# Kernel optimization log

Hardware: AMD Instinct MI355X
Metric: run time of the kernel (lower is better)

## Reference

```python
import jax, jax.numpy as jnp
import numpy as np

D_MODEL = 1024
N_HEADS = 16
D_HEAD = D_MODEL // N_HEADS
EPS = 1e-5


def setup_inputs() -> dict:
    key = jax.random.key(0)
    ks = jax.random.split(key, 7)
    B, T = 4, 2048
    s = 1.0 / np.sqrt(D_MODEL)
    return {
        "x": jax.random.normal(ks[0], (B, T, D_MODEL), dtype=jnp.float32),
        "ln_g": jnp.ones((D_MODEL,), jnp.float32),
        "ln_b": jnp.zeros((D_MODEL,), jnp.float32),
        "W_qkv": jax.random.normal(ks[1], (D_MODEL, 3 * D_MODEL), jnp.float32) * s,
        "b_qkv": jnp.zeros((3 * D_MODEL,), jnp.float32),
        "W_gate": jax.random.normal(ks[2], (D_MODEL, D_MODEL), jnp.float32) * s,
        "b_gate": jnp.zeros((D_MODEL,), jnp.float32),
        "W_proj": jax.random.normal(ks[3], (D_MODEL, D_MODEL), jnp.float32) * s,
        "b_proj": jnp.zeros((D_MODEL,), jnp.float32),
    }


def _forward(x, ln_g, ln_b, W_qkv, b_qkv, W_gate, b_gate, W_proj, b_proj):
    B, T, D = x.shape
    H, d = N_HEADS, D_HEAD
    # LayerNorm (eps=1e-5, biased variance as in torch)
    mu = jnp.mean(x, axis=-1, keepdims=True)
    var = jnp.mean((x - mu) ** 2, axis=-1, keepdims=True)
    x_norm = (x - mu) * jax.lax.rsqrt(var + EPS) * ln_g + ln_b
    qkv = x_norm @ W_qkv + b_qkv
    q, k, v = jnp.split(qkv, 3, axis=-1)  # each [B,T,D]
    # concept gate uses raw x
    gate = jax.nn.sigmoid(x @ W_gate + b_gate)
    gate = gate / (jnp.mean(gate, axis=-1, keepdims=True) + EPS)
    q = (q * gate).reshape(B, T, H, d)
    k = (k * gate).reshape(B, T, H, d)
    v = v.reshape(B, T, H, d)
    # ReLU^2 feature map in fp32
    q = jax.nn.relu(q.astype(jnp.float32)) ** 2 + EPS
    k = jax.nn.relu(k.astype(jnp.float32)) ** 2 + EPS
    v = v.astype(jnp.float32)
    # causal linear attention via kv recurrence (scan over T, T-major)
    qT = jnp.transpose(q, (1, 0, 2, 3))  # [T,B,H,d]
    kT = jnp.transpose(k, (1, 0, 2, 3))
    vT = jnp.transpose(v, (1, 0, 2, 3))

    def step(carry, inp):
        kv_s, k_s = carry  # [B,H,d,d], [B,H,d]
        q_t, k_t, v_t = inp  # [B,H,d]
        kv_s = kv_s + k_t[..., :, None] * v_t[..., None, :]
        k_s = k_s + k_t
        num = jnp.einsum('bhd,bhdm->bhm', q_t, kv_s)
        den = jnp.einsum('bhd,bhd->bh', q_t, k_s)[..., None] + EPS
        return (kv_s, k_s), num / den

    init = (jnp.zeros((B, H, d, d), jnp.float32), jnp.zeros((B, H, d), jnp.float32))
    _, outT = jax.lax.scan(step, init, (qT, kT, vT))  # [T,B,H,d]
    out = jnp.transpose(outT, (1, 0, 2, 3)).astype(x.dtype).reshape(B, T, D)
    return out @ W_proj + b_proj


def reference(x, ln_g, ln_b, W_qkv, b_qkv, W_gate, b_gate, W_proj, b_proj):
    return _forward(x, ln_g, ln_b, W_qkv, b_qkv, W_gate, b_gate, W_proj, b_proj)
```

## Files before the change

### kernel.cpp

```cpp
#include <hip/hip_runtime.h>
#include <math.h>

#define TOK 8192
#define DM 1024
#define EPSF 1e-5f

typedef __attribute__((ext_vector_type(8))) short short8;
typedef __attribute__((ext_vector_type(4))) float f32x4;

static __device__ __forceinline__ ushort f2bf(float f) {
  unsigned u = __float_as_uint(f);
  unsigned r = (u + 0x7fffu + ((u >> 16) & 1u)) >> 16;
  return (ushort)r;
}
static __device__ __forceinline__ float bf2f(ushort u) {
  return __uint_as_float((unsigned)u << 16);
}

static __device__ __forceinline__ void gload_lds16(const ushort* g, ushort* l) {
  __builtin_amdgcn_global_load_lds((const __attribute__((address_space(1))) void*)g,
                                   (__attribute__((address_space(3))) void*)l, 16, 0, 0);
}

static __device__ __forceinline__ int cswz(int row) {
  return (((row & 7) ^ ((row >> 3) & 7)) << 3);
}

__global__ __launch_bounds__(256) void lncvt_k(const float* __restrict__ x,
                                               const float* __restrict__ g,
                                               const float* __restrict__ b,
                                               ushort* __restrict__ x_b,
                                               ushort* __restrict__ xn_b) {
  __shared__ float red[8];
  int row = blockIdx.x;
  const float4* xr = (const float4*)(x + (size_t)row * DM);
  float4 v = xr[threadIdx.x];
  ushort4 xb4;
  xb4.x = f2bf(v.x); xb4.y = f2bf(v.y); xb4.z = f2bf(v.z); xb4.w = f2bf(v.w);
  ((ushort4*)(x_b + (size_t)row * DM))[threadIdx.x] = xb4;
  float s = v.x + v.y + v.z + v.w;
#pragma unroll
  for (int o = 32; o > 0; o >>= 1) s += __shfl_down(s, o, 64);
  int lane = threadIdx.x & 63, w = threadIdx.x >> 6;
  if (lane == 0) red[w] = s;
  __syncthreads();
  float mu = (red[0] + red[1] + red[2] + red[3]) * (1.0f / DM);
  float dx = v.x - mu, dy = v.y - mu, dz = v.z - mu, dw = v.w - mu;
  float ss = dx * dx + dy * dy + dz * dz + dw * dw;
#pragma unroll
  for (int o = 32; o > 0; o >>= 1) ss += __shfl_down(ss, o, 64);
  if (lane == 0) red[4 + w] = ss;
  __syncthreads();
  float var = (red[4] + red[5] + red[6] + red[7]) * (1.0f / DM);
  float rstd = rsqrtf(var + EPSF);
  float4 gg = ((const float4*)g)[threadIdx.x];
  float4 bb = ((const float4*)b)[threadIdx.x];
  ushort4 o4;
  o4.x = f2bf(dx * rstd * gg.x + bb.x);
  o4.y = f2bf(dy * rstd * gg.y + bb.y);
  o4.z = f2bf(dz * rstd * gg.z + bb.z);
  o4.w = f2bf(dw * rstd * gg.w + bb.w);
  ((ushort4*)(xn_b + (size_t)row * DM))[threadIdx.x] = o4;
}

__global__ __launch_bounds__(256) void tconv_all_k(
    const float* __restrict__ Wg, const float* __restrict__ Wq,
    const float* __restrict__ Wp, ushort* __restrict__ Wtg,
    ushort* __restrict__ Wtq, ushort* __restrict__ Wtp) {
  __shared__ ushort tile[32][33];
  int bid = blockIdx.x;
  const float* W; ushort* Wt; int N; int local;
  if (bid < 1024)      { W = Wg; Wt = Wtg; N = 1024; local = bid; }
  else if (bid < 4096) { W = Wq; Wt = Wtq; N = 3072; local = bid - 1024; }
  else                 { W = Wp; Wt = Wtp; N = 1024; local = bid - 4096; }
  int ntiles = N >> 5;
  int n0 = (local % ntiles) * 32, k0 = (local / ntiles) * 32;
  int tx = threadIdx.x & 31, ty = threadIdx.x >> 5;
#pragma unroll
  for (int i = 0; i < 4; i++) {
    int k = ty + i * 8;
    tile[k][tx] = f2bf(W[(size_t)(k0 + k) * N + n0 + tx]);
  }
  __syncthreads();
#pragma unroll
  for (int i = 0; i < 4; i++) {
    int n = ty + i * 8;
    Wt[(size_t)(n0 + n) * 1024 + k0 + tx] = tile[tx][n];
  }
}

__global__ __launch_bounds__(256) void rowinv_k(const ushort* __restrict__ gate_b,
                                                float* __restrict__ ginv) {
  int row = blockIdx.x * 4 + (threadIdx.x >> 6);
  int l = threadIdx.x & 63;
  const short8* gr = (const short8*)(gate_b + (size_t)row * DM);
  short8 g0 = gr[l * 2], g1 = gr[l * 2 + 1];
  float s = 0.f;
#pragma unroll
  for (int j = 0; j < 8; j++) s += bf2f((ushort)g0[j]) + bf2f((ushort)g1[j]);
#pragma unroll
  for (int o = 1; o < 64; o <<= 1) s += __shfl_xor(s, o, 64);
  if (l == 0) ginv[row] = 1.0f / (s * (1.0f / DM) + EPSF);
}

#define BM 128
#define BN 128
#define BK 64

static __device__ __forceinline__ void stage_tile128(
    const ushort* __restrict__ A, const ushort* __restrict__ Bt,
    int m0, int n0, int k0, int K, ushort* As, ushort* Bs, int w, int lane) {
#pragma unroll
  for (int j = 0; j < 4; j++) {
    int lu = (w * 4 + j) * 64 + lane;
    int r = lu >> 3;
    int kb = (lu & 7) ^ (r & 7);
    gload_lds16(A + (size_t)(m0 + r) * K + k0 + kb * 8, As + (w * 4 + j) * 512);
    gload_lds16(Bt + (size_t)(n0 + r) * K + k0 + kb * 8, Bs + (w * 4 + j) * 512);
  }
}

static __device__ __forceinline__ void compute_tile128(
    const ushort* as, const ushort* bs, int wr, int wc, int lane, f32x4 acc[4][4]) {
#pragma unroll
  for (int ks = 0; ks < 2; ks++) {
    short8 af[4], bfr[4];
    int kq = ks * 4 + (lane >> 4);
#pragma unroll
    for (int f = 0; f < 4; f++) {
      int ra = wr * 64 + f * 16 + (lane & 15);
      af[f] = *(const short8*)&as[(ra * 8 + (kq ^ (ra & 7))) * 8];
      int rb = wc * 64 + f * 16 + (lane & 15);
      bfr[f] = *(const short8*)&bs[(rb * 8 + (kq ^ (rb & 7))) * 8];
    }
#pragma unroll
    for (int i = 0; i < 4; i++)
#pragma unroll
      for (int j2 = 0; j2 < 4; j2++)
        acc[i][j2] = __builtin_amdgcn_mfma_f32_16x16x32_bf16(af[i], bfr[j2], acc[i][j2], 0, 0, 0);
  }
}

#define GEMM_LOOP128(A_, B_, m0_, n0_, K_)                                       \
  f32x4 acc[4][4] = {};                                                          \
  stage_tile128(A_, B_, m0_, n0_, 0, K_, sh, sh + 16384, w, lane);               \
  int nt = (K_) / BK;                                                            \
  for (int t = 0; t < nt; t++) {                                                 \
    __syncthreads();                                                             \
    if (t + 1 < nt)                                                              \
      stage_tile128(A_, B_, m0_, n0_, (t + 1) * BK, K_,                          \
                    sh + ((t + 1) & 1) * 8192, sh + 16384 + ((t + 1) & 1) * 8192,\
                    w, lane);                                                    \
    compute_tile128(sh + (t & 1) * 8192, sh + 16384 + (t & 1) * 8192,            \
                    wr, wc, lane, acc);                                          \
  }                                                                              \
  __syncthreads();

__global__ __launch_bounds__(256) void gemm_bf16_k(
    const ushort* __restrict__ A, const ushort* __restrict__ Bt,
    const float* __restrict__ bias, float* __restrict__ Cf,
    ushort* __restrict__ Cb, int ldc, int K, int mode) {
  __shared__ __align__(16) ushort sh[32768];
  int tid = threadIdx.x, lane = tid & 63, w = tid >> 6;
  int m0 = blockIdx.y * BM, n0 = blockIdx.x * BN;
  int wr = w >> 1, wc = w & 1;
  GEMM_LOOP128(A, Bt, m0, n0, K)
#pragma unroll
  for (int i = 0; i < 4; i++) {
#pragma unroll
    for (int j2 = 0; j2 < 4; j2++) {
      int col = n0 + wc * 64 + j2 * 16 + (lane & 15);
      float bv = bias[col];
#pragma unroll
      for (int r = 0; r < 4; r++) {
        int row = m0 + wr * 64 + i * 16 + (lane >> 4) * 4 + r;
        float v = acc[i][j2][r] + bv;
        if (mode == 2) {
          v = 1.0f / (1.0f + __expf(-v));
          Cb[(size_t)row * ldc + col] = f2bf(v);
        } else {
          Cf[(size_t)row * ldc + col] = v;
        }
      }
    }
  }
}

__global__ __launch_bounds__(256) void gemm_qkv_k(
    const ushort* __restrict__ A, const ushort* __restrict__ Bt,
    const float* __restrict__ bias, const ushort* __restrict__ gate_b,
    const float* __restrict__ ginv,
    ushort* __restrict__ qb, ushort* __restrict__ kb,
    ushort* __restrict__ kt, ushort* __restrict__ vt, int K) {
  __shared__ __align__(16) ushort sh[32768];
  __shared__ float ginvs[128];
  int tid = threadIdx.x, lane = tid & 63, w = tid >> 6;
  int m0 = blockIdx.y * BM, n0 = blockIdx.x * BN;
  int wr = w >> 1, wc = w & 1;
  GEMM_LOOP128(A, Bt, m0, n0, K)
  int region = n0 >> 10;
  int n0b = n0 & 1023;
  int h0 = n0b >> 6;
  if (region < 2) {
    if (tid < 128) ginvs[tid] = ginv[m0 + tid];
#pragma unroll
    for (int it = 0; it < 8; it++) {
      int e = it * 256 + tid;
      int row = e >> 4, ch = e & 15;
      *(short8*)&sh[row * 132 + ch * 8] =
          *(const short8*)&gate_b[(size_t)(m0 + row) * DM + n0b + ch * 8];
    }
    __syncthreads();
#pragma unroll
    for (int i = 0; i < 4; i++) {
#pragma unroll
      for (int j2 = 0; j2 < 4; j2++) {
        int cl = wc * 64 + j2 * 16 + (lane & 15);
        float bv = bias[n0 + cl];
        int rl0 = wr * 64 + i * 16 + (lane >> 4) * 4;
#pragma unroll
        for (int r = 0; r < 4; r++) {
          float gv = bf2f(sh[(rl0 + r) * 132 + cl]) * ginvs[rl0 + r];
          float v = (acc[i][j2][r] + bv) * gv;
          v = fmaxf(v, 0.0f);
          acc[i][j2][r] = v * v + EPSF;
        }
      }
    }
    __syncthreads();
  } else {
#pragma unroll
    for (int i = 0; i < 4; i++)
#pragma unroll
      for (int j2 = 0; j2 < 4; j2++) {
        int cl = wc * 64 + j2 * 16 + (lane & 15);
        float bv = bias[n0 + cl];
#pragma unroll
        for (int r = 0; r < 4; r++) acc[i][j2][r] += bv;
      }
  }
#pragma unroll
  for (int i = 0; i < 4; i++) {
#pragma unroll
    for (int j2 = 0; j2 < 4; j2++) {
      int cl = wc * 64 + j2 * 16 + (lane & 15);
      int rl0 = wr * 64 + i * 16 + (lane >> 4) * 4;
#pragma unroll
      for (int r = 0; r < 4; r++) {
        int row = rl0 + r;
        sh[row * 128 + (cl ^ cswz(row))] = f2bf(acc[i][j2][r]);
      }
    }
  }
  __syncthreads();
  if (region < 2) {
    ushort* dstRM = (region == 0) ? qb : kb;
#pragma unroll
    for (int it = 0; it < 8; it++) {
      int e = it * 256 + tid;
      int row = e >> 4, ch = e & 15;
      short8 val = *(const short8*)&sh[row * 128 + ((ch * 8) ^ cswz(row))];
      int tglob = m0 + row;
      size_t bh2 = (size_t)(tglob >> 11) * 16 + h0 + (ch >> 3);
      *(short8*)&dstRM[(bh2 * 2048 + (tglob & 2047)) * 64 + (ch & 7) * 8] = val;
    }
  }
  if (region >= 1) {
    ushort* dstT = (region == 1) ? kt : vt;
#pragma unroll
    for (int it = 0; it < 8; it++) {
      int e = it * 256 + tid;
      int tch = e & 15, dkrow = e >> 4;
      short8 val;
#pragma unroll
      for (int j = 0; j < 8; j++) {
        int row = tch * 8 + j;
        val[j] = (short)sh[row * 128 + (dkrow ^ cswz(row))];
      }
      int tglob0 = m0 + tch * 8;
      size_t bh2 = (size_t)(tglob0 >> 11) * 16 + h0 + (dkrow >> 6);
      *(short8*)&dstT[(bh2 * 64 + (dkrow & 63)) * 2048 + (tglob0 & 2047)] = val;
    }
  }
}

__global__ __launch_bounds__(256) void chunkpfx_k(const ushort* __restrict__ kt,
                                                  const ushort* __restrict__ vt,
                                                  ushort* __restrict__ KVb,
                                                  float* __restrict__ ksum) {
  int bid = blockIdx.x;
  int bh = (bid & 7) | ((bid >> 5) << 3);
  int dvs = (bid >> 3) & 3;
  int tid = threadIdx.x, l = tid & 63, w = tid >> 6;
  int lg = l >> 4;
  const ushort* vT = vt + ((size_t)bh * 64 + dvs * 16 + (l & 15)) * 2048;
  const ushort* kT = kt + ((size_t)bh * 64 + w * 16 + (l & 15)) * 2048;
  f32x4 run = {0.f, 0.f, 0.f, 0.f};
  float runks = 0.0f;
  short8 a0 = *(const short8*)&vT[lg * 8];
  short8 a1 = *(const short8*)&vT[32 + lg * 8];
  short8 b0 = *(const short8*)&kT[lg * 8];
  short8 b1 = *(const short8*)&kT[32 + lg * 8];
  for (int c = 0; c < 32; c++) {
    ushort* dst = KVb + ((size_t)bh * 32 + c) * 4096 +
                  (size_t)(dvs * 16 + lg * 4) * 64 + w * 16 + (l & 15);
    dst[0] = f2bf(run[0]); dst[64] = f2bf(run[1]);
    dst[128] = f2bf(run[2]); dst[192] = f2bf(run[3]);
    if (dvs == 0) {
      float s = 0.f;
#pragma unroll
      for (int j = 0; j < 8; j++) s += bf2f((ushort)b0[j]) + bf2f((ushort)b1[j]);
      s += __shfl_xor(s, 16, 64);
      s += __shfl_xor(s, 32, 64);
      if (l < 16) ksum[((size_t)bh * 32 + c) * 64 + w * 16 + l] = runks;
      runks += s;
    }
    int cn = (c + 1) & 31;
    short8 na0 = *(const short8*)&vT[cn * 64 + lg * 8];
    short8 na1 = *(const short8*)&vT[cn * 64 + 32 + lg * 8];
    short8 nb0 = *(const short8*)&kT[cn * 64 + lg * 8];
    short8 nb1 = *(const short8*)&kT[cn * 64 + 32 + lg * 8];
    run = __builtin_amdgcn_mfma_f32_16x16x32_bf16(a0, b0, run, 0, 0, 0);
    run = __builtin_amdgcn_mfma_f32_16x16x32_bf16(a1, b1, run, 0, 0, 0);
    a0 = na0; a1 = na1; b0 = nb0; b1 = nb1;
  }
}

__global__ __launch_bounds__(256) void attn_k(
    const ushort* __restrict__ qb, const ushort* __restrict__ kb,
    const ushort* __restrict__ vt, const ushort* __restrict__ KVb,
    const float* __restrict__ ks, ushort* __restrict__ attnout) {
  int c = blockIdx.x, bh = blockIdx.y;
  int b = bh >> 4, h = bh & 15;
  const ushort* qB = qb + ((size_t)bh * 2048 + (size_t)c * 64) * 64;
  const ushort* kB = kb + ((size_t)bh * 2048 + (size_t)c * 64) * 64;
  const ushort* vT = vt + (size_t)bh * 64 * 2048 + (size_t)c * 64;
  const ushort* kvB = KVb + ((size_t)bh * 32 + c) * 4096;
  const float* ksP = ks + ((size_t)bh * 32 + c) * 64;
  __shared__ __align__(16) char SL[64 * 128];
  __shared__ float denp[4][64];
  __shared__ float den2p[4][64];
  __shared__ float invden[64];
  int tid = threadIdx.x, l = tid & 63, w = tid >> 6;
  int lr = l & 15, lg = l >> 4;
  {
    short8 q0 = *(const short8*)&qB[(size_t)l * 64 + w * 16];
    short8 q1 = *(const short8*)&qB[(size_t)l * 64 + w * 16 + 8];
    float d2 = 0.0f;
#pragma unroll
    for (int j = 0; j < 8; j++) {
      d2 += bf2f((ushort)q0[j]) * ksP[w * 16 + j];
      d2 += bf2f((ushort)q1[j]) * ksP[w * 16 + 8 + j];
    }
    den2p[w][l] = d2;
  }
#pragma unroll
  for (int n = 0; n < 4; n++) {
    f32x4 sa = {0.f, 0.f, 0.f, 0.f};
#pragma unroll
    for (int g = 0; g < 2; g++) {
      short8 a = *(const short8*)&kB[(size_t)(w * 16 + lr) * 64 + g * 32 + lg * 8];
      short8 bq = *(const short8*)&qB[(size_t)(n * 16 + lr) * 64 + g * 32 + lg * 8];
      sa = __builtin_amdgcn_mfma_f32_16x16x32_bf16(a, bq, sa, 0, 0, 0);
    }
    int t = n * 16 + lr;
    int s0 = w * 16 + lg * 4;
    float dsum = 0.0f;
    ushort sb[4];
#pragma unroll
    for (int r = 0; r < 4; r++) {
      float v = (s0 + r <= t) ? sa[r] : 0.0f;
      dsum += v;
      sb[r] = f2bf(v);
    }
    dsum += __shfl_xor(dsum, 16, 64);
    dsum += __shfl_xor(dsum, 32, 64);
    if (l < 16) denp[w][n * 16 + l] = dsum;
    int u = (s0 >> 3) ^ (t & 7);
    uint2 p;
    p.x = sb[0] | ((unsigned)sb[1] << 16);
    p.y = sb[2] | ((unsigned)sb[3] << 16);
    *(uint2*)&SL[t * 128 + u * 16 + (s0 & 7) * 2] = p;
  }
  __syncthreads();
  if (tid < 64) {
    float den = denp[0][tid] + denp[1][tid] + denp[2][tid] + denp[3][tid] +
                den2p[0][tid] + den2p[1][tid] + den2p[2][tid] + den2p[3][tid] + EPSF;
    invden[tid] = 1.0f / den;
  }
  __syncthreads();
#pragma unroll
  for (int n = 0; n < 4; n++) {
    f32x4 oa = {0.f, 0.f, 0.f, 0.f};
#pragma unroll
    for (int g = 0; g < 2; g++) {
      short8 a = *(const short8*)&kvB[(size_t)(w * 16 + lr) * 64 + g * 32 + lg * 8];
      short8 bq = *(const short8*)&qB[(size_t)(n * 16 + lr) * 64 + g * 32 + lg * 8];
      oa = __builtin_amdgcn_mfma_f32_16x16x32_bf16(a, bq, oa, 0, 0, 0);
    }
    int t = n * 16 + lr;
#pragma unroll
    for (int g = 0; g < 2; g++) {
      short8 a = *(const short8*)&vT[(size_t)(w * 16 + lr) * 2048 + g * 32 + lg * 8];
      int u = (g * 4 + lg) ^ (t & 7);
      short8 bs = *(const short8*)&SL[t * 128 + u * 16];
      oa = __builtin_amdgcn_mfma_f32_16x16x32_bf16(a, bs, oa, 0, 0, 0);
    }
    float iv = invden[t];
    ushort ob[4];
#pragma unroll
    for (int r = 0; r < 4; r++) ob[r] = f2bf(oa[r] * iv);
    size_t tok = (size_t)b * 2048 + (size_t)c * 64 + t;
    uint2 p;
    p.x = ob[0] | ((unsigned)ob[1] << 16);
    p.y = ob[2] | ((unsigned)ob[3] << 16);
    *(uint2*)&attnout[tok * 1024 + h * 64 + w * 16 + lg * 4] = p;
  }
}

extern "C" void kernel_launch(void* const* d_in, const int* in_sizes, int n_in,
                              void* d_out, int out_size, void* d_ws, size_t ws_size,
                              hipStream_t stream) {
  const float* x      = (const float*)d_in[0];
  const float* ln_g   = (const float*)d_in[1];
  const float* ln_b   = (const float*)d_in[2];
  const float* W_qkv  = (const float*)d_in[3];
  const float* b_qkv  = (const float*)d_in[4];
  const float* W_gate = (const float*)d_in[5];
  const float* b_gate = (const float*)d_in[6];
  const float* W_proj = (const float*)d_in[7];
  const float* b_proj = (const float*)d_in[8];
  float* out = (float*)d_out;

  char* wsb = (char*)d_ws;
  const size_t TD = (size_t)TOK * DM;
  const size_t SLOT = TD * 2;
  ushort* x_b     = (ushort*)(wsb + 0 * SLOT);
  ushort* attnout = (ushort*)(wsb + 0 * SLOT);
  ushort* xn_b    = (ushort*)(wsb + 1 * SLOT);
  ushort* qb      = (ushort*)(wsb + 2 * SLOT);
  ushort* kb      = (ushort*)(wsb + 3 * SLOT);
  ushort* kt      = (ushort*)(wsb + 4 * SLOT);
  ushort* vt      = (ushort*)(wsb + 5 * SLOT);
  ushort* gate_b  = (ushort*)(wsb + 6 * SLOT);
  ushort* Wt_qkv  = (ushort*)(wsb + 8 * SLOT);
  ushort* Wt_gate = (ushort*)(wsb + 8 * SLOT + (size_t)8 * 1024 * 1024);
  ushort* KVb     = (ushort*)(wsb + 8 * SLOT);
  ushort* Wt_proj = (ushort*)(wsb + 9 * SLOT);
  float*  ksum    = (float*)(wsb + 9 * SLOT + (size_t)8 * 1024 * 1024);
  float*  ginv    = (float*)(wsb + 9 * SLOT + (size_t)12 * 1024 * 1024);

  lncvt_k<<<TOK, 256, 0, stream>>>(x, ln_g, ln_b, x_b, xn_b);
  tconv_all_k<<<5120, 256, 0, stream>>>(W_gate, W_qkv, W_proj, Wt_gate, Wt_qkv, Wt_proj);
  gemm_bf16_k<<<dim3(DM / BN, TOK / BM), 256, 0, stream>>>(x_b, Wt_gate, b_gate, nullptr,
                                                           gate_b, DM, DM, 2);
  rowinv_k<<<TOK / 4, 256, 0, stream>>>(gate_b, ginv);
  gemm_qkv_k<<<dim3(3 * DM / BN, TOK / BM), 256, 0, stream>>>(xn_b, Wt_qkv, b_qkv, gate_b,
                                                              ginv, qb, kb, kt, vt, DM);
  chunkpfx_k<<<256, 256, 0, stream>>>(kt, vt, KVb, ksum);
  attn_k<<<dim3(32, 64), 256, 0, stream>>>(qb, kb, vt, KVb, ksum, attnout);
  gemm_bf16_k<<<dim3(DM / BN, TOK / BM), 256, 0, stream>>>(attnout, Wt_proj, b_proj, out,
                                                           nullptr, DM, DM, 0);
}
```

Before: 194.8 us.

## Merge prep kernels and fuse gate row-sum into gate GEMM epilogue

Combines the layernorm/convert kernel and the weight transpose kernel into one launch. It also removes the separate row-inverse kernel: the gate GEMM epilogue now reduces partial row sums of the sigmoid outputs per column block into a small buffer, and the QKV GEMM sums the 8 partials to form the inverse mean. This drops two launches and a re-read of the bf16 gate matrix. In exchange it adds shuffle and LDS reduction work to the gate GEMM epilogue, and the sum is now taken over fp32 sigmoid values rather than bf16-rounded ones.

```diff
diff --git a/kernel.cpp b/kernel.cpp
--- a/kernel.cpp
+++ b/kernel.cpp
@@ -26,81 +26,66 @@
   return (((row & 7) ^ ((row >> 3) & 7)) << 3);
 }
 
-__global__ __launch_bounds__(256) void lncvt_k(const float* __restrict__ x,
-                                               const float* __restrict__ g,
-                                               const float* __restrict__ b,
-                                               ushort* __restrict__ x_b,
-                                               ushort* __restrict__ xn_b) {
-  __shared__ float red[8];
-  int row = blockIdx.x;
-  const float4* xr = (const float4*)(x + (size_t)row * DM);
-  float4 v = xr[threadIdx.x];
-  ushort4 xb4;
-  xb4.x = f2bf(v.x); xb4.y = f2bf(v.y); xb4.z = f2bf(v.z); xb4.w = f2bf(v.w);
-  ((ushort4*)(x_b + (size_t)row * DM))[threadIdx.x] = xb4;
-  float s = v.x + v.y + v.z + v.w;
-#pragma unroll
-  for (int o = 32; o > 0; o >>= 1) s += __shfl_down(s, o, 64);
-  int lane = threadIdx.x & 63, w = threadIdx.x >> 6;
-  if (lane == 0) red[w] = s;
-  __syncthreads();
-  float mu = (red[0] + red[1] + red[2] + red[3]) * (1.0f / DM);
-  float dx = v.x - mu, dy = v.y - mu, dz = v.z - mu, dw = v.w - mu;
-  float ss = dx * dx + dy * dy + dz * dz + dw * dw;
-#pragma unroll
-  for (int o = 32; o > 0; o >>= 1) ss += __shfl_down(ss, o, 64);
-  if (lane == 0) red[4 + w] = ss;
-  __syncthreads();
-  float var = (red[4] + red[5] + red[6] + red[7]) * (1.0f / DM);
-  float rstd = rsqrtf(var + EPSF);
-  float4 gg = ((const float4*)g)[threadIdx.x];
-  float4 bb = ((const float4*)b)[threadIdx.x];
-  ushort4 o4;
-  o4.x = f2bf(dx * rstd * gg.x + bb.x);
-  o4.y = f2bf(dy * rstd * gg.y + bb.y);
-  o4.z = f2bf(dz * rstd * gg.z + bb.z);
-  o4.w = f2bf(dw * rstd * gg.w + bb.w);
-  ((ushort4*)(xn_b + (size_t)row * DM))[threadIdx.x] = o4;
-}
-
-__global__ __launch_bounds__(256) void tconv_all_k(
+__global__ __launch_bounds__(256) void prep_k(
+    const float* __restrict__ x, const float* __restrict__ g,
+    const float* __restrict__ b, ushort* __restrict__ x_b,
+    ushort* __restrict__ xn_b,
     const float* __restrict__ Wg, const float* __restrict__ Wq,
     const float* __restrict__ Wp, ushort* __restrict__ Wtg,
     ushort* __restrict__ Wtq, ushort* __restrict__ Wtp) {
   __shared__ ushort tile[32][33];
-  int bid = blockIdx.x;
-  const float* W; ushort* Wt; int N; int local;
-  if (bid < 1024)      { W = Wg; Wt = Wtg; N = 1024; local = bid; }
-  else if (bid < 4096) { W = Wq; Wt = Wtq; N = 3072; local = bid - 1024; }
-  else                 { W = Wp; Wt = Wtp; N = 1024; local = bid - 4096; }
-  int ntiles = N >> 5;
-  int n0 = (local % ntiles) * 32, k0 = (local / ntiles) * 32;
-  int tx = threadIdx.x & 31, ty = threadIdx.x >> 5;
-#pragma unroll
-  for (int i = 0; i < 4; i++) {
-    int k = ty + i * 8;
-    tile[k][tx] = f2bf(W[(size_t)(k0 + k) * N + n0 + tx]);
-  }
-  __syncthreads();
-#pragma unroll
-  for (int i = 0; i < 4; i++) {
-    int n = ty + i * 8;
-    Wt[(size_t)(n0 + n) * 1024 + k0 + tx] = tile[tx][n];
-  }
-}
-
-__global__ __launch_bounds__(256) void rowinv_k(const ushort* __restrict__ gate_b,
-                                                float* __restrict__ ginv) {
-  int row = blockIdx.x * 4 + (threadIdx.x >> 6);
-  int l = threadIdx.x & 63;
-  const short8* gr = (const short8*)(gate_b + (size_t)row * DM);
-  short8 g0 = gr[l * 2], g1 = gr[l * 2 + 1];
-  float s = 0.f;
-#pragma unroll
-  for (int j = 0; j < 8; j++) s += bf2f((ushort)g0[j]) + bf2f((ushort)g1[j]);
-#pragma unroll
-  for (int o = 1; o < 64; o <<= 1) s += __shfl_xor(s, o, 64);
-  if (l == 0) ginv[row] = 1.0f / (s * (1.0f / DM) + EPSF);
+  __shared__ float red[8];
+  if (blockIdx.x < 8192) {
+    int row = blockIdx.x;
+    const float4* xr = (const float4*)(x + (size_t)row * DM);
+    float4 v = xr[threadIdx.x];
+    ushort4 xb4;
+    xb4.x = f2bf(v.x); xb4.y = f2bf(v.y); xb4.z = f2bf(v.z); xb4.w = f2bf(v.w);
+    ((ushort4*)(x_b + (size_t)row * DM))[threadIdx.x] = xb4;
+    float s = v.x + v.y + v.z + v.w;
+#pragma unroll
+    for (int o = 32; o > 0; o >>= 1) s += __shfl_down(s, o, 64);
+    int lane = threadIdx.x & 63, w = threadIdx.x >> 6;
+    if (lane == 0) red[w] = s;
+    __syncthreads();
+    float mu = (red[0] + red[1] + red[2] + red[3]) * (1.0f / DM);
+    float dx = v.x - mu, dy = v.y - mu, dz = v.z - mu, dw = v.w - mu;
+    float ss = dx * dx + dy * dy + dz * dz + dw * dw;
+#pragma unroll
+    for (int o = 32; o > 0; o >>= 1) ss += __shfl_down(ss, o, 64);
+    if (lane == 0) red[4 + w] = ss;
+    __syncthreads();
+    float var = (red[4] + red[5] + red[6] + red[7]) * (1.0f / DM);
+    float rstd = rsqrtf(var + EPSF);
+    float4 gg = ((const float4*)g)[threadIdx.x];
+    float4 bb = ((const float4*)b)[threadIdx.x];
+    ushort4 o4;
+    o4.x = f2bf(dx * rstd * gg.x + bb.x);
+    o4.y = f2bf(dy * rstd * gg.y + bb.y);
+    o4.z = f2bf(dz * rstd * gg.z + bb.z);
+    o4.w = f2bf(dw * rstd * gg.w + bb.w);
+    ((ushort4*)(xn_b + (size_t)row * DM))[threadIdx.x] = o4;
+  } else {
+    int bid = blockIdx.x - 8192;
+    const float* W; ushort* Wt; int N; int local;
+    if (bid < 1024)      { W = Wg; Wt = Wtg; N = 1024; local = bid; }
+    else if (bid < 4096) { W = Wq; Wt = Wtq; N = 3072; local = bid - 1024; }
+    else                 { W = Wp; Wt = Wtp; N = 1024; local = bid - 4096; }
+    int ntiles = N >> 5;
+    int n0 = (local % ntiles) * 32, k0 = (local / ntiles) * 32;
+    int tx = threadIdx.x & 31, ty = threadIdx.x >> 5;
+#pragma unroll
+    for (int i = 0; i < 4; i++) {
+      int k = ty + i * 8;
+      tile[k][tx] = f2bf(W[(size_t)(k0 + k) * N + n0 + tx]);
+    }
+    __syncthreads();
+#pragma unroll
+    for (int i = 0; i < 4; i++) {
+      int n = ty + i * 8;
+      Wt[(size_t)(n0 + n) * 1024 + k0 + tx] = tile[tx][n];
+    }
+  }
 }
 
 #define BM 128
@@ -158,8 +143,7 @@
 
 __global__ __launch_bounds__(256) void gemm_bf16_k(
     const ushort* __restrict__ A, const ushort* __restrict__ Bt,
-    const float* __restrict__ bias, float* __restrict__ Cf,
-    ushort* __restrict__ Cb, int ldc, int K, int mode) {
+    const float* __restrict__ bias, float* __restrict__ Cf, int ldc, int K) {
   __shared__ __align__(16) ushort sh[32768];
   int tid = threadIdx.x, lane = tid & 63, w = tid >> 6;
   int m0 = blockIdx.y * BM, n0 = blockIdx.x * BN;
@@ -174,22 +158,50 @@
 #pragma unroll
       for (int r = 0; r < 4; r++) {
         int row = m0 + wr * 64 + i * 16 + (lane >> 4) * 4 + r;
-        float v = acc[i][j2][r] + bv;
-        if (mode == 2) {
-          v = 1.0f / (1.0f + __expf(-v));
-          Cb[(size_t)row * ldc + col] = f2bf(v);
-        } else {
-          Cf[(size_t)row * ldc + col] = v;
-        }
-      }
-    }
-  }
+        Cf[(size_t)row * ldc + col] = acc[i][j2][r] + bv;
+      }
+    }
+  }
+}
+
+__global__ __launch_bounds__(256) void gemm_gate_k(
+    const ushort* __restrict__ A, const ushort* __restrict__ Bt,
+    const float* __restrict__ bias, ushort* __restrict__ Cb, int ldc, int K,
+    float* __restrict__ gpart) {
+  __shared__ __align__(16) ushort sh[32768];
+  int tid = threadIdx.x, lane = tid & 63, w = tid >> 6;
+  int m0 = blockIdx.y * BM, n0 = blockIdx.x * BN;
+  int wr = w >> 1, wc = w & 1;
+  GEMM_LOOP128(A, Bt, m0, n0, K)
+  int lr = lane & 15, lg = lane >> 4;
+  float* rs2 = (float*)sh;
+#pragma unroll
+  for (int i = 0; i < 4; i++) {
+#pragma unroll
+    for (int r = 0; r < 4; r++) {
+      float rsum = 0.0f;
+      int row = m0 + wr * 64 + i * 16 + lg * 4 + r;
+#pragma unroll
+      for (int j2 = 0; j2 < 4; j2++) {
+        int col = n0 + wc * 64 + j2 * 16 + lr;
+        float v = 1.0f / (1.0f + __expf(-(acc[i][j2][r] + bias[col])));
+        rsum += v;
+        Cb[(size_t)row * ldc + col] = f2bf(v);
+      }
+#pragma unroll
+      for (int o = 1; o < 16; o <<= 1) rsum += __shfl_xor(rsum, o, 64);
+      if (lr == 0) rs2[wc * 128 + wr * 64 + i * 16 + lg * 4 + r] = rsum;
+    }
+  }
+  __syncthreads();
+  if (tid < 128)
+    gpart[(size_t)(m0 + tid) * 8 + blockIdx.x] = rs2[tid] + rs2[128 + tid];
 }
 
 __global__ __launch_bounds__(256) void gemm_qkv_k(
     const ushort* __restrict__ A, const ushort* __restrict__ Bt,
     const float* __restrict__ bias, const ushort* __restrict__ gate_b,
-    const float* __restrict__ ginv,
+    const float* __restrict__ gpart,
     ushort* __restrict__ qb, ushort* __restrict__ kb,
     ushort* __restrict__ kt, ushort* __restrict__ vt, int K) {
   __shared__ __align__(16) ushort sh[32768];
@@ -202,7 +214,12 @@
   int n0b = n0 & 1023;
   int h0 = n0b >> 6;
   if (region < 2) {
-    if (tid < 128) ginvs[tid] = ginv[m0 + tid];
+    if (tid < 128) {
+      const float4* gp = (const float4*)&gpart[(size_t)(m0 + tid) * 8];
+      float4 s0 = gp[0], s1 = gp[1];
+      float s = s0.x + s0.y + s0.z + s0.w + s1.x + s1.y + s1.z + s1.w;
+      ginvs[tid] = 1.0f / (s * (1.0f / DM) + EPSF);
+    }
 #pragma unroll
     for (int it = 0; it < 8; it++) {
       int e = it * 256 + tid;
@@ -448,17 +465,17 @@
   ushort* KVb     = (ushort*)(wsb + 8 * SLOT);
   ushort* Wt_proj = (ushort*)(wsb + 9 * SLOT);
   float*  ksum    = (float*)(wsb + 9 * SLOT + (size_t)8 * 1024 * 1024);
-  float*  ginv    = (float*)(wsb + 9 * SLOT + (size_t)12 * 1024 * 1024);
-
-  lncvt_k<<<TOK, 256, 0, stream>>>(x, ln_g, ln_b, x_b, xn_b);
-  tconv_all_k<<<5120, 256, 0, stream>>>(W_gate, W_qkv, W_proj, Wt_gate, Wt_qkv, Wt_proj);
-  gemm_bf16_k<<<dim3(DM / BN, TOK / BM), 256, 0, stream>>>(x_b, Wt_gate, b_gate, nullptr,
-                                                           gate_b, DM, DM, 2);
-  rowinv_k<<<TOK / 4, 256, 0, stream>>>(gate_b, ginv);
+  float*  gpart   = (float*)(wsb + 9 * SLOT + (size_t)12 * 1024 * 1024);
+
+  prep_k<<<8192 + 5120, 256, 0, stream>>>(x, ln_g, ln_b, x_b, xn_b,
+                                          W_gate, W_qkv, W_proj,
+                                          Wt_gate, Wt_qkv, Wt_proj);
+  gemm_gate_k<<<dim3(DM / BN, TOK / BM), 256, 0, stream>>>(x_b, Wt_gate, b_gate,
+                                                           gate_b, DM, DM, gpart);
   gemm_qkv_k<<<dim3(3 * DM / BN, TOK / BM), 256, 0, stream>>>(xn_b, Wt_qkv, b_qkv, gate_b,
-                                                              ginv, qb, kb, kt, vt, DM);
+                                                              gpart, qb, kb, kt, vt, DM);
   chunkpfx_k<<<256, 256, 0, stream>>>(kt, vt, KVb, ksum);
   attn_k<<<dim3(32, 64), 256, 0, stream>>>(qb, kb, vt, KVb, ksum, attnout);
   gemm_bf16_k<<<dim3(DM / BN, TOK / BM), 256, 0, stream>>>(attnout, Wt_proj, b_proj, out,
-                                                           nullptr, DM, DM, 0);
-}
+                                                           DM, DM);
+}
```

Result: faster. 187.0 us (-4.0%).
